# Kernel tuning notes

Measured on AMD Instinct MI355X. Metric: run time of the kernel, lower is better.

The kernel has to match this reference:

```python
import jax, jax.numpy as jnp
import numpy as np

# Tree config: batch of perfect binary trees in heap layout (root=0, children of i are 2i+1, 2i+2)
D_MODEL = 512
DEPTH = 10                      # number of internal levels
B = 64                          # number of trees in the batch
VOCAB = 32000
N_LEAVES = 2 ** DEPTH           # 1024 leaves per tree
N_NODES = 2 ** (DEPTH + 1) - 1  # 2047 nodes per tree
N_CLASSES = 2                   # binary graph classification


def setup_inputs() -> dict:
    key = jax.random.key(0)
    k_tok, k_emb, k_iou, k_f, k_out = jax.random.split(key, 5)
    d = D_MODEL
    s_in = 1.0 / np.sqrt(2 * d)
    return {
        "tokens": jax.random.randint(k_tok, (B, N_LEAVES), 0, VOCAB, dtype=jnp.int32),
        "embedding": (jax.random.normal(k_emb, (VOCAB, d), jnp.float32) * 0.02),
        "W_iou": jax.random.normal(k_iou, (2 * d, 3 * d), jnp.float32) * s_in,
        "b_iou": jnp.zeros((3 * d,), jnp.float32),
        "W_f": jax.random.normal(k_f, (2 * d, 2 * d), jnp.float32) * s_in,
        "b_f": jnp.zeros((2 * d,), jnp.float32),
        "W_out": jax.random.normal(k_out, (d, N_CLASSES), jnp.float32) * (1.0 / np.sqrt(d)),
    }


def reference(tokens, embedding, W_iou, b_iou, W_f, b_f, W_out):
    # Shared activation / memory buffers over all nodes, as in RecursiveNN.forward.
    d = embedding.shape[1]
    b = tokens.shape[0]
    h = jnp.zeros((b, N_NODES, d), jnp.float32)   # activations
    c = jnp.zeros((b, N_NODES, d), jnp.float32)   # memory (memory_size=1)

    # Leaves: embedding lookup, scattered into the activation buffer.
    leaf_h = embedding[tokens]                    # [B, N_LEAVES, d]
    h = h.at[:, N_LEAVES - 1:].set(leaf_h)

    # Internal nodes by topological level (leaf-adjacent level first, root last).
    for level in range(DEPTH - 1, -1, -1):
        idx = np.arange(2 ** level - 1, 2 ** (level + 1) - 1)  # node group (static)
        left, right = 2 * idx + 1, 2 * idx + 2                 # predecessor indices
        # Gather predecessor activations and memory.
        hl, hr = h[:, left], h[:, right]                       # [B, n, d]
        cl, cr = c[:, left], c[:, right]
        x = jnp.concatenate([hl, hr], axis=-1)                 # [B, n, 2d]
        # Binary TreeLSTM cell (the _apply_function for the 'add' binary op).
        iou = x @ W_iou + b_iou
        i, o, u = jnp.split(iou, 3, axis=-1)
        f = jax.nn.sigmoid(x @ W_f + b_f)
        fl, fr = jnp.split(f, 2, axis=-1)
        c_new = jax.nn.sigmoid(i) * jnp.tanh(u) + fl * cl + fr * cr
        h_new = jax.nn.sigmoid(o) * jnp.tanh(c_new)
        # Scatter back into the shared buffers.
        h = h.at[:, idx].set(h_new)
        c = c.at[:, idx].set(c_new)

    # _compute_output: linear binary-classification head on the root activation.
    return h[:, 0] @ W_out                                     # [B, N_CLASSES]
```

## Files before the change

kernel.cpp:

```cpp
#include <hip/hip_runtime.h>
#include <math.h>

typedef unsigned short u16;
typedef short s16x8 __attribute__((ext_vector_type(8)));
typedef float f32x4 __attribute__((ext_vector_type(4)));

#define NITER 32
#define ARW 72

__device__ __align__(16) u16 g_Bhi[1024 * 2560];
__device__ __align__(16) u16 g_Blo[1024 * 2560];
__device__ __align__(16) u16 g_Aleaf[(size_t)64 * 1024 * 1024];

__device__ __forceinline__ u16 f2bf(float x) {
    unsigned u = __float_as_uint(x);
    u += 0x7fffu + ((u >> 16) & 1u);
    return (u16)(u >> 16);
}
__device__ __forceinline__ float bf2f(u16 h) { return __uint_as_float(((unsigned)h) << 16); }
__device__ __forceinline__ float sigm(float x) { return 1.0f / (1.0f + expf(-x)); }
__device__ __forceinline__ unsigned pk(u16 a, u16 b) { return (unsigned)a | ((unsigned)b << 16); }

__device__ __forceinline__ void gload16(const void* g, u16* l) {
    __builtin_amdgcn_global_load_lds(
        (const __attribute__((address_space(1))) void*)g,
        (__attribute__((address_space(3))) void*)(void*)l, 16, 0, 0);
}

__global__ __launch_bounds__(256)
void wsplit_kernel(const float* __restrict__ Wiou, const float* __restrict__ Wf)
{
    __shared__ float tile[32][65];
    const int kb = blockIdx.x;
    const int cb = blockIdx.y;
    const int t  = threadIdx.x;
    const int c0 = cb * 64;

    {
        const int kk  = t >> 3;
        const int cu0 = (t & 7) * 8;
        const int k   = kb * 32 + kk;
#pragma unroll
        for (int u = 0; u < 8; u++) {
            int c = c0 + cu0 + u;
            float v = (c < 1536) ? Wiou[(size_t)k * 1536 + c]
                                 : Wf[(size_t)k * 1024 + (c - 1536)];
            tile[kk][cu0 + u] = v;
        }
    }
    __syncthreads();
    {
        const int jl = t >> 2;
        const int kc = (t & 3) * 8;
        const int g  = c0 >> 9;
        const int j  = (c0 & 511) + jl;
        size_t dst = (((size_t)kb * 5 + g) * 512 + j) * 32 + kc;
        unsigned ph[4], pl[4];
#pragma unroll
        for (int u = 0; u < 4; u++) {
            float v0 = tile[kc + 2 * u][jl];
            float v1 = tile[kc + 2 * u + 1][jl];
            u16 h0 = f2bf(v0), h1 = f2bf(v1);
            u16 l0 = f2bf(v0 - bf2f(h0)), l1 = f2bf(v1 - bf2f(h1));
            ph[u] = pk(h0, h1);
            pl[u] = pk(l0, l1);
        }
        *(uint4*)(g_Bhi + dst) = make_uint4(ph[0], ph[1], ph[2], ph[3]);
        *(uint4*)(g_Blo + dst) = make_uint4(pl[0], pl[1], pl[2], pl[3]);
    }
}

__global__ __launch_bounds__(256)
void leafgather_kernel(const int* __restrict__ tokens, const float* __restrict__ emb)
{
    const int gidx = blockIdx.x * 256 + threadIdx.x;
    const int row  = gidx >> 5;
    const int c    = gidx & 31;
    const int tok  = tokens[row];
    const float* src = emb + (size_t)tok * 512 + c * 16;
    u16* dst = g_Aleaf + (size_t)row * 1024 + c * 32;

    float4 f0 = *(const float4*)(src);
    float4 f1 = *(const float4*)(src + 4);
    float4 f2 = *(const float4*)(src + 8);
    float4 f3 = *(const float4*)(src + 12);
    float v[16] = {f0.x,f0.y,f0.z,f0.w, f1.x,f1.y,f1.z,f1.w,
                   f2.x,f2.y,f2.z,f2.w, f3.x,f3.y,f3.z,f3.w};
    unsigned ph[8], pl[8];
#pragma unroll
    for (int i = 0; i < 8; i++) {
        u16 h0 = f2bf(v[2*i]),   h1 = f2bf(v[2*i+1]);
        u16 l0 = f2bf(v[2*i]   - bf2f(h0));
        u16 l1 = f2bf(v[2*i+1] - bf2f(h1));
        ph[i] = pk(h0, h1);
        pl[i] = pk(l0, l1);
    }
    *(uint4*)(dst)      = make_uint4(ph[0], ph[1], ph[2], ph[3]);
    *(uint4*)(dst + 8)  = make_uint4(ph[4], ph[5], ph[6], ph[7]);
    *(uint4*)(dst + 16) = make_uint4(pl[0], pl[1], pl[2], pl[3]);
    *(uint4*)(dst + 24) = make_uint4(pl[4], pl[5], pl[6], pl[7]);
}

template<bool LEAF>
__global__ __launch_bounds__(256, 2)
void level_big(const u16* __restrict__ Hcin, const float* __restrict__ Cc,
               const float* __restrict__ b_iou, const float* __restrict__ b_f,
               u16* __restrict__ Hp, float* __restrict__ Cp,
               int np, int lgnp)
{
    __shared__ __align__(16) u16 Ab0[4096];
    __shared__ __align__(16) u16 Ab1[4096];

    const u16* Hc = LEAF ? g_Aleaf : Hcin;

    const int tid = threadIdx.x;
    const int jg  = blockIdx.x;
    const int m0  = blockIdx.y * 64;
    const int j0  = jg * 64;
    const int nc  = np * 2;

    const int w    = tid >> 6;
    const int lane = tid & 63;
    const int il   = lane & 15;
    const int kq   = lane >> 4;
    const int wc   = w;

    f32x4 acc[4][5];
#pragma unroll
    for (int rf = 0; rf < 4; rf++)
#pragma unroll
        for (int g = 0; g < 5; g++) acc[rf][g] = (f32x4)0.0f;

    const int bA  = m0 >> lgnp;
    const int pA0 = m0 & (np - 1);
    const char* A0u = (const char*)(Hc + ((size_t)bA * nc + 2 * pA0) * 1024);
    const int rowS = tid >> 3;
    const int segS = (tid & 7) ^ (rowS & 7);
    const unsigned voffA = (unsigned)rowS * 4096u + (unsigned)segS * 16u;
    u16* d00 = Ab0 + w * 512;
    u16* d01 = Ab0 + 2048 + w * 512;
    u16* d10 = Ab1 + w * 512;
    u16* d11 = Ab1 + 2048 + w * 512;

    const int shi = ((kq >> 1) << 2) | (kq & 1);
    const int x7  = il & 7;
    const int aoh = il * 64 + ((shi ^ x7) * 8);
    const int aol = il * 64 + (((shi + 2) ^ x7) * 8);

    const char* BH0 = (const char*)(g_Bhi + (size_t)j0 * 32);
    const char* BL0 = (const char*)(g_Blo + (size_t)j0 * 32);
    unsigned vB[5];
#pragma unroll
    for (int g = 0; g < 5; g++)
        vB[g] = (unsigned)(((wc * 16 + il) * 32 + kq * 8) * 2 + g * 32768);

    s16x8 b0h[5], b0l[5], b1h[5], b1l[5];

#define STAGEA(D0, D1, t_)                                                     \
    {                                                                          \
        const char* ab = A0u + (size_t)(t_) * 128;                             \
        gload16(ab + voffA, D0);                                               \
        gload16(ab + 131072 + voffA, D1);                                      \
    }

#define LOADB_HI(BH, t_)                                                       \
    {                                                                          \
        const char* bh = BH0 + (size_t)(t_) * 163840;                          \
        _Pragma("unroll")                                                      \
        for (int g = 0; g < 5; g++) BH[g] = *(const s16x8*)(bh + vB[g]);       \
    }

#define LOADB_LO(BL, t_)                                                       \
    {                                                                          \
        const char* bl = BL0 + (size_t)(t_) * 163840;                          \
        _Pragma("unroll")                                                      \
        for (int g = 0; g < 5; g++) BL[g] = *(const s16x8*)(bl + vB[g]);       \
    }

#define MFMA_PASS(AREGS, BSET)                                                 \
    {                                                                          \
        __builtin_amdgcn_s_setprio(1);                                         \
        _Pragma("unroll")                                                      \
        for (int rf = 0; rf < 4; rf++)                                         \
            _Pragma("unroll")                                                  \
            for (int g = 0; g < 5; g++)                                        \
                acc[rf][g] = __builtin_amdgcn_mfma_f32_16x16x32_bf16(AREGS[rf], BSET[g], acc[rf][g], 0, 0, 0); \
        __builtin_amdgcn_s_setprio(0);                                         \
    }

#define TILE_BODY(AB, BHc, BLc, BHn, BLn, t_, more_)                           \
    {                                                                          \
        if (more_) {                                                           \
            STAGEA((AB == Ab0 ? d10 : d00), (AB == Ab0 ? d11 : d01), (t_) + 1);\
            __builtin_amdgcn_sched_barrier(0);                                 \
        }                                                                      \
        s16x8 ah[4], al[4];                                                    \
        _Pragma("unroll")                                                      \
        for (int rf = 0; rf < 4; rf++) {                                       \
            ah[rf] = *(const s16x8*)&AB[aoh + rf * 1024];                      \
            al[rf] = *(const s16x8*)&AB[aol + rf * 1024];                      \
        }                                                                      \
        MFMA_PASS(ah, BHc);                                                    \
        if (more_) LOADB_HI(BHn, (t_) + 1);                                    \
        MFMA_PASS(ah, BLc);                                                    \
        if (more_) LOADB_LO(BLn, (t_) + 1);                                    \
        MFMA_PASS(al, BHc);                                                    \
        if (more_) {                                                           \
            asm volatile("s_waitcnt vmcnt(10)" ::: "memory");                  \
            __builtin_amdgcn_s_barrier();                                      \
            __builtin_amdgcn_sched_barrier(0);                                 \
        }                                                                      \
    }

    STAGEA(d00, d01, 0);
    __builtin_amdgcn_sched_barrier(0);
    LOADB_HI(b0h, 0);
    LOADB_LO(b0l, 0);
    asm volatile("s_waitcnt vmcnt(10)" ::: "memory");
    __builtin_amdgcn_s_barrier();
    __builtin_amdgcn_sched_barrier(0);

#pragma unroll 1
    for (int t = 0; t < NITER; t += 2) {
        TILE_BODY(Ab0, b0h, b0l, b1h, b1l, t, (t + 1 < NITER));
        TILE_BODY(Ab1, b1h, b1l, b0h, b0l, t + 1, (t + 2 < NITER));
    }
#undef STAGEA
#undef LOADB_HI
#undef LOADB_LO
#undef MFMA_PASS
#undef TILE_BODY

    const int jglob = j0 + wc * 16 + il;
    const float bi  = b_iou[jglob];
    const float bo_ = b_iou[512 + jglob];
    const float bu  = b_iou[1024 + jglob];
    const float bfl = b_f[jglob];
    const float bfr = b_f[512 + jglob];

#pragma unroll
    for (int rf = 0; rf < 4; rf++) {
#pragma unroll
        for (int r = 0; r < 4; r++) {
            const int m  = m0 + rf * 16 + kq * 4 + r;
            const int b  = m >> lgnp;
            const int p  = m & (np - 1);
            float i_ = acc[rf][0][r] + bi;
            float o_ = acc[rf][1][r] + bo_;
            float u_ = acc[rf][2][r] + bu;
            float fl = sigm(acc[rf][3][r] + bfl);
            float fr = sigm(acc[rf][4][r] + bfr);
            float cl = 0.0f, cr_ = 0.0f;
            if (!LEAF) {
                size_t cb_ = ((size_t)b * nc + 2 * p) * 512 + jglob;
                cl  = Cc[cb_];
                cr_ = Cc[cb_ + 512];
            }
            float cn = sigm(i_) * tanhf(u_) + fl * cl + fr * cr_;
            float hn = sigm(o_) * tanhf(cn);
            size_t prow = (size_t)b * np + p;
            u16 hh  = f2bf(hn);
            u16 hlo = f2bf(hn - bf2f(hh));
            Hp[prow * 1024 + (size_t)(jg * 4 + wc) * 32 + il]      = hh;
            Hp[prow * 1024 + (size_t)(jg * 4 + wc) * 32 + 16 + il] = hlo;
            Cp[prow * 512 + jglob] = cn;
        }
    }
}

__global__ __launch_bounds__(256, 2)
void level_small(const u16* __restrict__ Hc, const float* __restrict__ Cc,
                 const float* __restrict__ b_iou, const float* __restrict__ b_f,
                 u16* __restrict__ Hp, float* __restrict__ Cp,
                 int np, int lgnp)
{
    __shared__ __align__(16) u16 Ac[2][64 * ARW];

    const int tid = threadIdx.x;
    const int jg  = blockIdx.x;
    const int m0  = blockIdx.y * 64;
    const int j0  = jg * 64;
    const int nc  = np * 2;
    const int M   = np * 64;

    const int w    = tid >> 6;
    const int lane = tid & 63;
    const int il   = lane & 15;
    const int kq   = lane >> 4;
    const int wc   = w;

    f32x4 acc[4][5];
#pragma unroll
    for (int rf = 0; rf < 4; rf++)
#pragma unroll
        for (int g = 0; g < 5; g++) acc[rf][g] = (f32x4)0.0f;

    const int rA = tid >> 2;
    const int qA = tid & 3;
    int mA = m0 + rA; if (mA > M - 1) mA = M - 1;
    const int bA = mA >> lgnp;
    const int pA = mA & (np - 1);
    const u16* arow = Hc + ((size_t)bA * nc + 2 * pA) * 1024;
    const int daI = rA * ARW + (qA & 1) * 32 + (qA >> 1) * 16;

    const char* BH0 = (const char*)(g_Bhi + (size_t)j0 * 32);
    const char* BL0 = (const char*)(g_Blo + (size_t)j0 * 32);
    unsigned vB[5];
#pragma unroll
    for (int g = 0; g < 5; g++)
        vB[g] = (unsigned)(((wc * 16 + il) * 32 + kq * 8) * 2 + g * 32768);

    uint4  aR0, aR1;
    s16x8 b0h[5], b0l[5], b1h[5], b1l[5];

#define LOADA(t_)                                                              \
    {                                                                          \
        const u16* asrc = arow + (t_) * 64 + qA * 16;                          \
        aR0 = *(const uint4*)asrc;                                             \
        aR1 = *(const uint4*)(asrc + 8);                                       \
    }
#define LOADB(BH, BL, t_)                                                      \
    {                                                                          \
        const char* bh = BH0 + (size_t)(t_) * 163840;                          \
        const char* bl = BL0 + (size_t)(t_) * 163840;                          \
        _Pragma("unroll")                                                      \
        for (int g = 0; g < 5; g++) {                                          \
            BH[g] = *(const s16x8*)(bh + vB[g]);                               \
            BL[g] = *(const s16x8*)(bl + vB[g]);                               \
        }                                                                      \
    }
#define WRITEA(bf)                                                             \
    {                                                                          \
        *(uint4*)&Ac[bf][daI]     = aR0;                                       \
        *(uint4*)&Ac[bf][daI + 8] = aR1;                                       \
    }
#define COMPUTE(BH, BL, BUF)                                                   \
    {                                                                          \
        _Pragma("unroll")                                                      \
        for (int rf = 0; rf < 4; rf++) {                                       \
            const int ao = (rf * 16 + il) * ARW + kq * 8;                      \
            s16x8 ahv = *(const s16x8*)&Ac[BUF][ao];                           \
            s16x8 alv = *(const s16x8*)&Ac[BUF][ao + 32];                      \
            _Pragma("unroll")                                                  \
            for (int g = 0; g < 5; g++) {                                      \
                acc[rf][g] = __builtin_amdgcn_mfma_f32_16x16x32_bf16(ahv, BH[g], acc[rf][g], 0, 0, 0); \
                acc[rf][g] = __builtin_amdgcn_mfma_f32_16x16x32_bf16(ahv, BL[g], acc[rf][g], 0, 0, 0); \
                acc[rf][g] = __builtin_amdgcn_mfma_f32_16x16x32_bf16(alv, BH[g], acc[rf][g], 0, 0, 0); \
            }                                                                  \
        }                                                                      \
    }

    LOADA(0);
    LOADB(b0h, b0l, 0);
    WRITEA(0);
    __syncthreads();

#pragma unroll 1
    for (int t = 0; t < NITER; t += 2) {
        if (t + 1 < NITER) { LOADA(t + 1); LOADB(b1h, b1l, t + 1); }
        COMPUTE(b0h, b0l, 0);
        if (t + 1 < NITER) { WRITEA(1); __syncthreads(); }
        if (t + 2 < NITER) { LOADA(t + 2); LOADB(b0h, b0l, t + 2); }
        COMPUTE(b1h, b1l, 1);
        if (t + 2 < NITER) { WRITEA(0); __syncthreads(); }
    }
#undef LOADA
#undef LOADB
#undef WRITEA
#undef COMPUTE

    const int jglob = j0 + wc * 16 + il;
    const float bi  = b_iou[jglob];
    const float bo_ = b_iou[512 + jglob];
    const float bu  = b_iou[1024 + jglob];
    const float bfl = b_f[jglob];
    const float bfr = b_f[512 + jglob];

#pragma unroll
    for (int rf = 0; rf < 4; rf++) {
#pragma unroll
        for (int r = 0; r < 4; r++) {
            const int m = m0 + rf * 16 + kq * 4 + r;
            if (m < M) {
                const int b = m >> lgnp;
                const int p = m & (np - 1);
                float i_ = acc[rf][0][r] + bi;
                float o_ = acc[rf][1][r] + bo_;
                float u_ = acc[rf][2][r] + bu;
                float fl = sigm(acc[rf][3][r] + bfl);
                float fr = sigm(acc[rf][4][r] + bfr);
                size_t cb_ = ((size_t)b * nc + 2 * p) * 512 + jglob;
                float cl  = Cc[cb_];
                float cr_ = Cc[cb_ + 512];
                float cn = sigm(i_) * tanhf(u_) + fl * cl + fr * cr_;
                float hn = sigm(o_) * tanhf(cn);
                size_t prow = (size_t)b * np + p;
                u16 hh  = f2bf(hn);
                u16 hlo = f2bf(hn - bf2f(hh));
                Hp[prow * 1024 + (size_t)(jg * 4 + wc) * 32 + il]      = hh;
                Hp[prow * 1024 + (size_t)(jg * 4 + wc) * 32 + 16 + il] = hlo;
                Cp[prow * 512 + jglob] = cn;
            }
        }
    }
}

__global__ __launch_bounds__(256)
void out_kernel(const u16* __restrict__ Hroot, const float* __restrict__ W_out,
                float* __restrict__ out)
{
    const int b = blockIdx.x;
    const int tid = threadIdx.x;
    float s0 = 0.f, s1 = 0.f;
    for (int d = tid; d < 512; d += 256) {
        const u16* row = Hroot + (size_t)b * 1024 + (d >> 4) * 32 + (d & 15);
        float h = bf2f(row[0]) + bf2f(row[16]);
        s0 = fmaf(h, W_out[d * 2 + 0], s0);
        s1 = fmaf(h, W_out[d * 2 + 1], s1);
    }
#pragma unroll
    for (int off = 32; off > 0; off >>= 1) {
        s0 += __shfl_down(s0, off, 64);
        s1 += __shfl_down(s1, off, 64);
    }
    __shared__ float red[2][4];
    const int wave = tid >> 6;
    if ((tid & 63) == 0) { red[0][wave] = s0; red[1][wave] = s1; }
    __syncthreads();
    if (tid == 0) {
        float t0 = 0.f, t1 = 0.f;
#pragma unroll
        for (int wv = 0; wv < 4; wv++) { t0 += red[0][wv]; t1 += red[1][wv]; }
        out[b * 2 + 0] = t0;
        out[b * 2 + 1] = t1;
    }
}

extern "C" void kernel_launch(void* const* d_in, const int* in_sizes, int n_in,
                              void* d_out, int out_size, void* d_ws, size_t ws_size,
                              hipStream_t stream)
{
    const int*   tokens = (const int*)  d_in[0];
    const float* emb    = (const float*)d_in[1];
    const float* W_iou  = (const float*)d_in[2];
    const float* b_iou  = (const float*)d_in[3];
    const float* W_f    = (const float*)d_in[4];
    const float* b_f    = (const float*)d_in[5];
    const float* W_out  = (const float*)d_in[6];
    float* out = (float*)d_out;

    u16*   H0 = (u16*)d_ws;
    float* C0 = (float*)(H0 + (size_t)512 * 64 * 1024);
    u16*   H1 = (u16*)(C0 + (size_t)512 * 64 * 512);
    float* C1 = (float*)(H1 + (size_t)256 * 64 * 1024);

    wsplit_kernel<<<dim3(32, 40), 256, 0, stream>>>(W_iou, W_f);
    leafgather_kernel<<<8192, 256, 0, stream>>>(tokens, emb);

    level_big<true><<<dim3(8, 512), 256, 0, stream>>>(
        nullptr, nullptr, b_iou, b_f, H0, C0, 512, 9);

    u16* Hc = H0;  float* Cc = C0;
    u16* Hp = H1;  float* Cp = C1;
    for (int L = 8; L >= 0; L--) {
        const int np = 1 << L;
        if (np >= 64) {
            level_big<false><<<dim3(8, np), 256, 0, stream>>>(
                Hc, Cc, b_iou, b_f, Hp, Cp, np, L);
        } else {
            level_small<<<dim3(8, np), 256, 0, stream>>>(
                Hc, Cc, b_iou, b_f, Hp, Cp, np, L);
        }
        u16* tH = Hc; Hc = Hp; Hp = tH;
        float* tC = Cc; Cc = Cp; Cp = tC;
    }

    out_kernel<<<64, 256, 0, stream>>>(Hc, W_out, out);
}
```

Measured before the change: 1.287 ms.

## Single-buffer B fragments in registers and raise occupancy to three blocks

Replaces the double-buffered B fragment registers (current and next tile) with a single set. The MFMA passes are reordered so the hi fragments are fully consumed before the next tile's hi loads are issued, and likewise for the lo fragments. This frees register pressure, so launch bounds are raised from 2 to 3 blocks per SM to improve latency hiding. The cost is that B loads for the next tile have less compute to overlap with inside each wave, especially the lo load, which is now issued just before the wait.

```diff
diff --git a/kernel.cpp b/kernel.cpp
--- a/kernel.cpp
+++ b/kernel.cpp
@@ -102,7 +102,7 @@
 }
 
 template<bool LEAF>
-__global__ __launch_bounds__(256, 2)
+__global__ __launch_bounds__(256, 3)
 void level_big(const u16* __restrict__ Hcin, const float* __restrict__ Cc,
                const float* __restrict__ b_iou, const float* __restrict__ b_f,
                u16* __restrict__ Hp, float* __restrict__ Cp,
@@ -154,7 +154,7 @@
     for (int g = 0; g < 5; g++)
         vB[g] = (unsigned)(((wc * 16 + il) * 32 + kq * 8) * 2 + g * 32768);
 
-    s16x8 b0h[5], b0l[5], b1h[5], b1l[5];
+    s16x8 bh[5], bl[5];
 
 #define STAGEA(D0, D1, t_)                                                     \
     {                                                                          \
@@ -163,18 +163,18 @@
         gload16(ab + 131072 + voffA, D1);                                      \
     }
 
-#define LOADB_HI(BH, t_)                                                       \
-    {                                                                          \
-        const char* bh = BH0 + (size_t)(t_) * 163840;                          \
-        _Pragma("unroll")                                                      \
-        for (int g = 0; g < 5; g++) BH[g] = *(const s16x8*)(bh + vB[g]);       \
-    }
-
-#define LOADB_LO(BL, t_)                                                       \
-    {                                                                          \
-        const char* bl = BL0 + (size_t)(t_) * 163840;                          \
-        _Pragma("unroll")                                                      \
-        for (int g = 0; g < 5; g++) BL[g] = *(const s16x8*)(bl + vB[g]);       \
+#define LOADB_HI(t_)                                                           \
+    {                                                                          \
+        const char* bhp = BH0 + (size_t)(t_) * 163840;                         \
+        _Pragma("unroll")                                                      \
+        for (int g = 0; g < 5; g++) bh[g] = *(const s16x8*)(bhp + vB[g]);      \
+    }
+
+#define LOADB_LO(t_)                                                           \
+    {                                                                          \
+        const char* blp = BL0 + (size_t)(t_) * 163840;                         \
+        _Pragma("unroll")                                                      \
+        for (int g = 0; g < 5; g++) bl[g] = *(const s16x8*)(blp + vB[g]);      \
     }
 
 #define MFMA_PASS(AREGS, BSET)                                                 \
@@ -188,7 +188,7 @@
         __builtin_amdgcn_s_setprio(0);                                         \
     }
 
-#define TILE_BODY(AB, BHc, BLc, BHn, BLn, t_, more_)                           \
+#define TILE_BODY(AB, t_, more_)                                               \
     {                                                                          \
         if (more_) {                                                           \
             STAGEA((AB == Ab0 ? d10 : d00), (AB == Ab0 ? d11 : d01), (t_) + 1);\
@@ -200,12 +200,12 @@
             ah[rf] = *(const s16x8*)&AB[aoh + rf * 1024];                      \
             al[rf] = *(const s16x8*)&AB[aol + rf * 1024];                      \
         }                                                                      \
-        MFMA_PASS(ah, BHc);                                                    \
-        if (more_) LOADB_HI(BHn, (t_) + 1);                                    \
-        MFMA_PASS(ah, BLc);                                                    \
-        if (more_) LOADB_LO(BLn, (t_) + 1);                                    \
-        MFMA_PASS(al, BHc);                                                    \
+        MFMA_PASS(ah, bh);                                                     \
+        MFMA_PASS(al, bh);                                                     \
+        if (more_) LOADB_HI((t_) + 1);                                         \
+        MFMA_PASS(ah, bl);                                                     \
         if (more_) {                                                           \
+            LOADB_LO((t_) + 1);                                                \
             asm volatile("s_waitcnt vmcnt(10)" ::: "memory");                  \
             __builtin_amdgcn_s_barrier();                                      \
             __builtin_amdgcn_sched_barrier(0);                                 \
@@ -214,16 +214,16 @@
 
     STAGEA(d00, d01, 0);
     __builtin_amdgcn_sched_barrier(0);
-    LOADB_HI(b0h, 0);
-    LOADB_LO(b0l, 0);
+    LOADB_HI(0);
+    LOADB_LO(0);
     asm volatile("s_waitcnt vmcnt(10)" ::: "memory");
     __builtin_amdgcn_s_barrier();
     __builtin_amdgcn_sched_barrier(0);
 
 #pragma unroll 1
     for (int t = 0; t < NITER; t += 2) {
-        TILE_BODY(Ab0, b0h, b0l, b1h, b1l, t, (t + 1 < NITER));
-        TILE_BODY(Ab1, b1h, b1l, b0h, b0l, t + 1, (t + 2 < NITER));
+        TILE_BODY(Ab0, t, (t + 1 < NITER));
+        TILE_BODY(Ab1, t + 1, (t + 2 < NITER));
     }
 #undef STAGEA
 #undef LOADB_HI
```

Result: slower. 4.855 ms (+277.3%).

## Halve level_big block to two waves covering 32 output columns

Applied to the files above, without the earlier changes.

Splits each level_big block into two 128-thread blocks, each computing 32 hidden columns instead of 64, with each thread staging four A chunks into LDS instead of two. This doubles the block count and is meant to raise occupancy and parallelism on the big levels. In exchange each A tile is loaded from global memory twice as often, since two blocks now share the same rows, and each block has fewer waves to hide latency.

```diff
diff --git a/kernel.cpp b/kernel.cpp
--- a/kernel.cpp
+++ b/kernel.cpp
@@ -102,7 +102,7 @@
 }
 
 template<bool LEAF>
-__global__ __launch_bounds__(256, 2)
+__global__ __launch_bounds__(128, 2)
 void level_big(const u16* __restrict__ Hcin, const float* __restrict__ Cc,
                const float* __restrict__ b_iou, const float* __restrict__ b_f,
                u16* __restrict__ Hp, float* __restrict__ Cp,
@@ -114,16 +114,14 @@
     const u16* Hc = LEAF ? g_Aleaf : Hcin;
 
     const int tid = threadIdx.x;
-    const int jg  = blockIdx.x;
+    const int sub = blockIdx.x;
     const int m0  = blockIdx.y * 64;
-    const int j0  = jg * 64;
     const int nc  = np * 2;
 
     const int w    = tid >> 6;
     const int lane = tid & 63;
     const int il   = lane & 15;
     const int kq   = lane >> 4;
-    const int wc   = w;
 
     f32x4 acc[4][5];
 #pragma unroll
@@ -134,47 +132,51 @@
     const int bA  = m0 >> lgnp;
     const int pA0 = m0 & (np - 1);
     const char* A0u = (const char*)(Hc + ((size_t)bA * nc + 2 * pA0) * 1024);
-    const int rowS = tid >> 3;
-    const int segS = (tid & 7) ^ (rowS & 7);
-    const unsigned voffA = (unsigned)rowS * 4096u + (unsigned)segS * 16u;
-    u16* d00 = Ab0 + w * 512;
-    u16* d01 = Ab0 + 2048 + w * 512;
-    u16* d10 = Ab1 + w * 512;
-    u16* d11 = Ab1 + 2048 + w * 512;
+    unsigned voff[4];
+#pragma unroll
+    for (int q = 0; q < 4; q++) {
+        const int u_   = q * 128 + tid;
+        const int rowq = u_ >> 3;
+        const int colq = u_ & 7;
+        const int ssrc = colq ^ (rowq & 7);
+        voff[q] = (unsigned)rowq * 4096u + (unsigned)ssrc * 16u;
+    }
 
     const int shi = ((kq >> 1) << 2) | (kq & 1);
     const int x7  = il & 7;
     const int aoh = il * 64 + ((shi ^ x7) * 8);
     const int aol = il * 64 + (((shi + 2) ^ x7) * 8);
 
-    const char* BH0 = (const char*)(g_Bhi + (size_t)j0 * 32);
-    const char* BL0 = (const char*)(g_Blo + (size_t)j0 * 32);
+    const char* BH0 = (const char*)(g_Bhi + (size_t)(sub * 32) * 32);
+    const char* BL0 = (const char*)(g_Blo + (size_t)(sub * 32) * 32);
     unsigned vB[5];
 #pragma unroll
     for (int g = 0; g < 5; g++)
-        vB[g] = (unsigned)(((wc * 16 + il) * 32 + kq * 8) * 2 + g * 32768);
+        vB[g] = (unsigned)(((w * 16 + il) * 32 + kq * 8) * 2 + g * 32768);
 
     s16x8 b0h[5], b0l[5], b1h[5], b1l[5];
 
-#define STAGEA(D0, D1, t_)                                                     \
+#define STAGEA(AB, t_)                                                         \
     {                                                                          \
         const char* ab = A0u + (size_t)(t_) * 128;                             \
-        gload16(ab + voffA, D0);                                               \
-        gload16(ab + 131072 + voffA, D1);                                      \
+        gload16(ab + voff[0], AB + w * 512);                                   \
+        gload16(ab + voff[1], AB + 1024 + w * 512);                            \
+        gload16(ab + voff[2], AB + 2048 + w * 512);                            \
+        gload16(ab + voff[3], AB + 3072 + w * 512);                            \
     }
 
 #define LOADB_HI(BH, t_)                                                       \
     {                                                                          \
-        const char* bh = BH0 + (size_t)(t_) * 163840;                          \
-        _Pragma("unroll")                                                      \
-        for (int g = 0; g < 5; g++) BH[g] = *(const s16x8*)(bh + vB[g]);       \
+        const char* bhp = BH0 + (size_t)(t_) * 163840;                         \
+        _Pragma("unroll")                                                      \
+        for (int g = 0; g < 5; g++) BH[g] = *(const s16x8*)(bhp + vB[g]);      \
     }
 
 #define LOADB_LO(BL, t_)                                                       \
     {                                                                          \
-        const char* bl = BL0 + (size_t)(t_) * 163840;                          \
-        _Pragma("unroll")                                                      \
-        for (int g = 0; g < 5; g++) BL[g] = *(const s16x8*)(bl + vB[g]);       \
+        const char* blp = BL0 + (size_t)(t_) * 163840;                         \
+        _Pragma("unroll")                                                      \
+        for (int g = 0; g < 5; g++) BL[g] = *(const s16x8*)(blp + vB[g]);      \
     }
 
 #define MFMA_PASS(AREGS, BSET)                                                 \
@@ -188,10 +190,10 @@
         __builtin_amdgcn_s_setprio(0);                                         \
     }
 
-#define TILE_BODY(AB, BHc, BLc, BHn, BLn, t_, more_)                           \
+#define TILE_BODY(AB, ABN, BHc, BLc, BHn, BLn, t_, more_)                      \
     {                                                                          \
         if (more_) {                                                           \
-            STAGEA((AB == Ab0 ? d10 : d00), (AB == Ab0 ? d11 : d01), (t_) + 1);\
+            STAGEA(ABN, (t_) + 1);                                             \
             __builtin_amdgcn_sched_barrier(0);                                 \
         }                                                                      \
         s16x8 ah[4], al[4];                                                    \
@@ -212,7 +214,7 @@
         }                                                                      \
     }
 
-    STAGEA(d00, d01, 0);
+    STAGEA(Ab0, 0);
     __builtin_amdgcn_sched_barrier(0);
     LOADB_HI(b0h, 0);
     LOADB_LO(b0l, 0);
@@ -222,8 +224,8 @@
 
 #pragma unroll 1
     for (int t = 0; t < NITER; t += 2) {
-        TILE_BODY(Ab0, b0h, b0l, b1h, b1l, t, (t + 1 < NITER));
-        TILE_BODY(Ab1, b1h, b1l, b0h, b0l, t + 1, (t + 2 < NITER));
+        TILE_BODY(Ab0, Ab1, b0h, b0l, b1h, b1l, t, (t + 1 < NITER));
+        TILE_BODY(Ab1, Ab0, b1h, b1l, b0h, b0l, t + 1, (t + 2 < NITER));
     }
 #undef STAGEA
 #undef LOADB_HI
@@ -231,12 +233,13 @@
 #undef MFMA_PASS
 #undef TILE_BODY
 
-    const int jglob = j0 + wc * 16 + il;
+    const int jglob = sub * 32 + w * 16 + il;
     const float bi  = b_iou[jglob];
     const float bo_ = b_iou[512 + jglob];
     const float bu  = b_iou[1024 + jglob];
     const float bfl = b_f[jglob];
     const float bfr = b_f[512 + jglob];
+    const int hchunk = sub * 2 + w;
 
 #pragma unroll
     for (int rf = 0; rf < 4; rf++) {
@@ -261,8 +264,8 @@
             size_t prow = (size_t)b * np + p;
             u16 hh  = f2bf(hn);
             u16 hlo = f2bf(hn - bf2f(hh));
-            Hp[prow * 1024 + (size_t)(jg * 4 + wc) * 32 + il]      = hh;
-            Hp[prow * 1024 + (size_t)(jg * 4 + wc) * 32 + 16 + il] = hlo;
+            Hp[prow * 1024 + (size_t)hchunk * 32 + il]      = hh;
+            Hp[prow * 1024 + (size_t)hchunk * 32 + 16 + il] = hlo;
             Cp[prow * 512 + jglob] = cn;
         }
     }
@@ -457,7 +460,7 @@
     wsplit_kernel<<<dim3(32, 40), 256, 0, stream>>>(W_iou, W_f);
     leafgather_kernel<<<8192, 256, 0, stream>>>(tokens, emb);
 
-    level_big<true><<<dim3(8, 512), 256, 0, stream>>>(
+    level_big<true><<<dim3(16, 512), 128, 0, stream>>>(
         nullptr, nullptr, b_iou, b_f, H0, C0, 512, 9);
 
     u16* Hc = H0;  float* Cc = C0;
@@ -465,7 +468,7 @@
     for (int L = 8; L >= 0; L--) {
         const int np = 1 << L;
         if (np >= 64) {
-            level_big<false><<<dim3(8, np), 256, 0, stream>>>(
+            level_big<false><<<dim3(16, np), 128, 0, stream>>>(
                 Hc, Cc, b_iou, b_f, Hp, Cp, np, L);
         } else {
             level_small<<<dim3(8, np), 256, 0, stream>>>(
```

Result: slower. 1.873 ms (+45.6%).
